# Performance work log

Measured on AMD Instinct MI355X. Metric: run time of the kernel, lower is better.

## Reference

```python
import jax, jax.numpy as jnp
import numpy as np

T = 131072          # signal length == RIR length
C = 4               # audio channels (torch code requires batch == 1)
SAMPLE_RATE = 16000
RT60 = 0.8          # 'large' room


def setup_inputs() -> dict:
    key = jax.random.key(0)
    k_audio, k_rir = jax.random.split(key)
    audio = jax.random.normal(k_audio, (1, C, T), dtype=jnp.float32)
    # synthetic RIR: exponentially decaying white noise, direct-path impulse at t=0
    t = jnp.arange(T, dtype=jnp.float32)
    decay = jnp.exp(-6.9 * t / (RT60 * SAMPLE_RATE))
    rir = jax.random.normal(k_rir, (T,), dtype=jnp.float32) * decay
    rir = rir.at[0].set(1.0)
    return {"audio": audio, "rir": rir}


def reference(audio, rir):
    # torch F.conv1d with padding = K-1 computes FULL cross-correlation:
    #   out[n] = sum_j audio[n-(K-1)+j] * rir[j],  n = 0..T+K-2
    # which equals full linear convolution of audio with flipped rir.
    # Implemented via zero-padded rFFT (mathematically identical, O(N log N)).
    L = audio.shape[-1] + rir.shape[-1] - 1          # 2T-1
    A = jnp.fft.rfft(audio, n=L, axis=-1)            # (1, C, Lf)
    K = jnp.fft.rfft(rir[::-1], n=L)                 # (Lf,)
    out = jnp.fft.irfft(A * K, n=L, axis=-1)         # (1, C, 2T-1)
    return out.astype(audio.dtype)
```

## Files before the change

kernel.cpp:

```cpp
#include <hip/hip_runtime.h>


#define NTOT 262144
#define TLEN 131072
#define PI2_N    2.3968449808418217e-5f
#define PI2_1024 6.1359231515425649e-3f
#define PI2_256  2.4543692606170260e-2f
#define LB(i) ((i) + ((i) >> 3))

__device__ __forceinline__ float2 cadd(float2 a, float2 b) { return make_float2(a.x + b.x, a.y + b.y); }
__device__ __forceinline__ float2 csub(float2 a, float2 b) { return make_float2(a.x - b.x, a.y - b.y); }
__device__ __forceinline__ float2 cmul(float2 a, float2 b) {
    return make_float2(a.x * b.x - a.y * b.y, a.x * b.y + a.y * b.x);
}
__device__ __forceinline__ float2 cmulc(float2 a, float2 b) {
    return make_float2(a.x * b.x + a.y * b.y, a.y * b.x - a.x * b.y);
}
__device__ __forceinline__ float2 cexp_(float ang) {
    float s, c;
    __sincosf(ang, &s, &c);
    return make_float2(c, s);
}

constexpr float CW16[16] = { 1.f, 0.92387953f, 0.70710678f, 0.38268343f, 0.f, -0.38268343f,
                             -0.70710678f, -0.92387953f, -1.f, -0.92387953f, -0.70710678f,
                             -0.38268343f, 0.f, 0.38268343f, 0.70710678f, 0.92387953f };
constexpr float SW16[16] = { 0.f, 0.38268343f, 0.70710678f, 0.92387953f, 1.f, 0.92387953f,
                             0.70710678f, 0.38268343f, 0.f, -0.38268343f, -0.70710678f,
                             -0.92387953f, -1.f, -0.92387953f, -0.70710678f, -0.38268343f };

template<int SIGN>
__device__ __forceinline__ void dft4(float2 x[4]) {
    float2 s0 = cadd(x[0], x[2]), d0 = csub(x[0], x[2]);
    float2 s1 = cadd(x[1], x[3]), d1 = csub(x[1], x[3]);
    float2 jd1 = (SIGN > 0) ? make_float2(-d1.y, d1.x) : make_float2(d1.y, -d1.x);
    x[0] = cadd(s0, s1);
    x[1] = cadd(d0, jd1);
    x[2] = csub(s0, s1);
    x[3] = csub(d0, jd1);
}

template<int SIGN, bool HZ>
__device__ __forceinline__ void dft16(float2 x[16]) {
    float2 A[4][4];
#pragma unroll
    for (int m0 = 0; m0 < 4; ++m0) {
        float2 g[4];
        if (HZ) {
            float2 a = x[m0], b = x[m0 + 4];
            float2 jb = (SIGN > 0) ? make_float2(-b.y, b.x) : make_float2(b.y, -b.x);
            g[0] = cadd(a, b);
            g[1] = cadd(a, jb);
            g[2] = csub(a, b);
            g[3] = csub(a, jb);
        } else {
            g[0] = x[m0]; g[1] = x[m0 + 4]; g[2] = x[m0 + 8]; g[3] = x[m0 + 12];
            dft4<SIGN>(g);
        }
#pragma unroll
        for (int j = 0; j < 4; ++j) {
            int k = (m0 * j) & 15;
            float2 w = make_float2(CW16[k], (SIGN < 0) ? -SW16[k] : SW16[k]);
            A[m0][j] = (m0 && j) ? cmul(g[j], w) : g[j];
        }
    }
#pragma unroll
    for (int j = 0; j < 4; ++j) {
        float2 g[4];
#pragma unroll
        for (int m0 = 0; m0 < 4; ++m0) g[m0] = A[m0][j];
        dft4<SIGN>(g);
#pragma unroll
        for (int l = 0; l < 4; ++l) x[j + 4 * l] = g[l];
    }
}

template<int SIGN>
__device__ __forceinline__ void twtab4(float2 x[4], int base, const float2* __restrict__ tab) {
#pragma unroll
    for (int i = 1; i < 4; ++i) {
        float2 w = tab[base * i];
        x[i] = (SIGN < 0) ? cmul(x[i], w) : cmulc(x[i], w);
    }
}

template<int SIGN>
__device__ void fft1024(float2 x[4], int t, float2* L0, float2* L1,
                        const float2* __restrict__ tab) {
    dft4<SIGN>(x);
    twtab4<SIGN>(x, t, tab);
#pragma unroll
    for (int i = 0; i < 4; ++i) L0[LB(4 * t + i)] = x[i];
    __syncthreads();
    {
        int q = t & 3, p = t >> 2;
#pragma unroll
        for (int i = 0; i < 4; ++i) x[i] = L0[LB(q + 4 * p + 256 * i)];
        dft4<SIGN>(x);
        twtab4<SIGN>(x, 4 * p, tab);
#pragma unroll
        for (int i = 0; i < 4; ++i) L1[LB(q + 16 * p + 4 * i)] = x[i];
    }
    __syncthreads();
    {
        int q = t & 15, p = t >> 4;
#pragma unroll
        for (int i = 0; i < 4; ++i) x[i] = L1[LB(q + 16 * p + 256 * i)];
        dft4<SIGN>(x);
        twtab4<SIGN>(x, 16 * p, tab);
#pragma unroll
        for (int i = 0; i < 4; ++i) L0[LB(q + 64 * p + 16 * i)] = x[i];
    }
    __syncthreads();
    {
        int q = t & 63, p = t >> 6;
#pragma unroll
        for (int i = 0; i < 4; ++i) x[i] = L0[LB(q + 64 * p + 256 * i)];
        dft4<SIGN>(x);
        twtab4<SIGN>(x, 64 * p, tab);
#pragma unroll
        for (int i = 0; i < 4; ++i) L1[LB(q + 256 * p + 64 * i)] = x[i];
    }
    __syncthreads();
#pragma unroll
    for (int i = 0; i < 4; ++i) x[i] = L1[LB(t + 256 * i)];
    dft4<SIGN>(x);
}

__global__ void __launch_bounds__(256) ka(const float* __restrict__ audio,
                                          const float* __restrict__ rir,
                                          float2* __restrict__ A1,
                                          float2* __restrict__ tab) {
    __shared__ float2 lds[256 * 17];
    const int bid = blockIdx.x;
    const int tid = threadIdx.x;
    const int c = tid & 15;
    const int t = tid >> 4;

    if (bid < 4)
        tab[bid * 256 + tid] = cexp_(-PI2_1024 * (float)(bid * 256 + tid));

    const int seq = bid >> 6;
    const int n2 = ((bid & 63) << 4) + c;

    float2 g[16];
    if (seq < 2) {
        const float* c0 = audio + (size_t)(2 * seq) * TLEN;
        const float* c1 = c0 + TLEN;
#pragma unroll
        for (int v = 0; v < 8; ++v) {
            int n = ((t + 16 * v) << 10) + n2;
            g[v] = make_float2(c0[n], c1[n]);
        }
    } else {
#pragma unroll
        for (int v = 0; v < 8; ++v) {
            int n = ((t + 16 * v) << 10) + n2;
            g[v] = make_float2(rir[TLEN - 1 - n], 0.f);
        }
    }

    dft16<-1, true>(g);
#pragma unroll
    for (int r = 1; r < 16; ++r)
        g[r] = cmul(g[r], cexp_(-PI2_256 * (float)(t * r)));
    if (t) g[0] = g[0];
#pragma unroll
    for (int r = 0; r < 16; ++r) lds[(r * 16 + t) * 17 + c] = g[r];
    __syncthreads();
#pragma unroll
    for (int u = 0; u < 16; ++u) g[u] = lds[(t * 16 + u) * 17 + c];

    dft16<-1, false>(g);

    float2* dst = A1 + ((size_t)seq << 18) + n2;
#pragma unroll
    for (int r = 0; r < 16; ++r) {
        int k1 = t + 16 * r;
        float2 v = cmul(g[r], cexp_(-PI2_N * (float)(n2 * k1)));
        dst[(size_t)k1 << 10] = v;
    }
}

__global__ void __launch_bounds__(256) kbf(const float2* __restrict__ A1,
                                           float2* __restrict__ Spec,
                                           const float2* __restrict__ tab) {
    __shared__ float2 L0[1152], L1[1152];
    const int t = threadIdx.x;
    const float2* src = A1 + ((size_t)blockIdx.x << 10);
    float2 x[4];
#pragma unroll
    for (int i = 0; i < 4; ++i) x[i] = src[t + 256 * i];
    fft1024<-1>(x, t, L0, L1, tab);
    float2* dst = Spec + ((size_t)blockIdx.x << 10) + t;
#pragma unroll
    for (int i = 0; i < 4; ++i) dst[256 * i] = x[i];
}

__global__ void __launch_bounds__(256) kbi(const float2* __restrict__ Spec,
                                           float2* __restrict__ D,
                                           const float2* __restrict__ tab) {
    __shared__ float2 L0[1152], L1[1152];
    const int t = threadIdx.x;
    const int k1 = blockIdx.x & 255;

    const float2* sz = Spec + ((size_t)blockIdx.x << 10);
    const float2* sr = Spec + ((size_t)(512 + k1) << 10);
    float2 x[4], r4[4];
#pragma unroll
    for (int i = 0; i < 4; ++i) x[i] = sz[t + 256 * i];
#pragma unroll
    for (int i = 0; i < 4; ++i) r4[i] = sr[t + 256 * i];

    const float invN = 3.814697265625e-6f;
#pragma unroll
    for (int i = 0; i < 4; ++i) {
        float2 y = cmul(x[i], r4[i]);
        x[i] = make_float2(y.x * invN, y.y * invN);
    }

    fft1024<1>(x, t, L0, L1, tab);

    float2 w  = cexp_(PI2_N * (float)(t * k1));
    float2 st = make_float2(tab[k1].x, -tab[k1].y);
    float2* d = D + ((size_t)blockIdx.x << 10) + t;
#pragma unroll
    for (int i = 0; i < 4; ++i) {
        d[256 * i] = cmul(x[i], w);
        w = cmul(w, st);
    }
}

__global__ void __launch_bounds__(256) kc(const float2* __restrict__ D,
                                          float* __restrict__ out, int Lout) {
    __shared__ float2 lds[256 * 17];
    const int bid = blockIdx.x;
    const int tid = threadIdx.x;
    const int c = tid & 15;
    const int t = tid >> 4;
    const int z = bid >> 6;
    const int n2 = ((bid & 63) << 4) + c;

    const float2* src = D + ((size_t)z << 18) + n2;
    float2 g[16];
#pragma unroll
    for (int v = 0; v < 16; ++v)
        g[v] = src[(size_t)(t + 16 * v) << 10];

    dft16<1, false>(g);
#pragma unroll
    for (int r = 1; r < 16; ++r)
        g[r] = cmul(g[r], cexp_(PI2_256 * (float)(t * r)));
#pragma unroll
    for (int r = 0; r < 16; ++r) lds[(r * 16 + t) * 17 + c] = g[r];
    __syncthreads();
#pragma unroll
    for (int u = 0; u < 16; ++u) g[u] = lds[(t * 16 + u) * 17 + c];

    dft16<1, false>(g);

    float* o0 = out + (size_t)(2 * z) * Lout;
    float* o1 = o0 + Lout;
#pragma unroll
    for (int r = 0; r < 16; ++r) {
        int n = ((t + 16 * r) << 10) + n2;
        if (n < Lout) { o0[n] = g[r].x; o1[n] = g[r].y; }
    }
}

extern "C" void kernel_launch(void* const* d_in, const int* in_sizes, int n_in,
                              void* d_out, int out_size, void* d_ws, size_t ws_size,
                              hipStream_t stream) {
    const float* audio = (const float*)d_in[0];
    const float* rir   = (const float*)d_in[1];
    float* out = (float*)d_out;
    int Lout = out_size / 4;

    float2* A1   = (float2*)d_ws;
    float2* Spec = A1 + 3 * NTOT;
    float2* D    = Spec + 3 * NTOT;
    float2* tab  = D + 2 * NTOT;

    ka <<<192, 256, 0, stream>>>(audio, rir, A1, tab);
    kbf<<<768, 256, 0, stream>>>(A1, Spec, tab);
    kbi<<<512, 256, 0, stream>>>(Spec, D, tab);
    kc <<<128, 256, 0, stream>>>(D, out, Lout);
}
```

Before: 24.83 us.

## Fuse forward column FFT into pointwise-multiply inverse FFT kernel

Merges the forward 1024-point FFT stage into the inverse-stage kernel. Each block now transforms its own audio row and the matching RIR row before multiplying, so the separate kernel launch and the Spec round trip through global memory go away. In exchange, the RIR row FFT is recomputed once per audio channel pair (twice per row instead of once), and each block does two more FFTs in sequence.

```diff
diff --git a/kernel.cpp b/kernel.cpp
--- a/kernel.cpp
+++ b/kernel.cpp
@@ -164,7 +164,6 @@
 #pragma unroll
     for (int r = 1; r < 16; ++r)
         g[r] = cmul(g[r], cexp_(-PI2_256 * (float)(t * r)));
-    if (t) g[0] = g[0];
 #pragma unroll
     for (int r = 0; r < 16; ++r) lds[(r * 16 + t) * 17 + c] = g[r];
     __syncthreads();
@@ -182,35 +181,23 @@
     }
 }
 
-__global__ void __launch_bounds__(256) kbf(const float2* __restrict__ A1,
-                                           float2* __restrict__ Spec,
-                                           const float2* __restrict__ tab) {
-    __shared__ float2 L0[1152], L1[1152];
-    const int t = threadIdx.x;
-    const float2* src = A1 + ((size_t)blockIdx.x << 10);
-    float2 x[4];
-#pragma unroll
-    for (int i = 0; i < 4; ++i) x[i] = src[t + 256 * i];
-    fft1024<-1>(x, t, L0, L1, tab);
-    float2* dst = Spec + ((size_t)blockIdx.x << 10) + t;
-#pragma unroll
-    for (int i = 0; i < 4; ++i) dst[256 * i] = x[i];
-}
-
-__global__ void __launch_bounds__(256) kbi(const float2* __restrict__ Spec,
-                                           float2* __restrict__ D,
-                                           const float2* __restrict__ tab) {
+__global__ void __launch_bounds__(256) kb(const float2* __restrict__ A1,
+                                          float2* __restrict__ D,
+                                          const float2* __restrict__ tab) {
     __shared__ float2 L0[1152], L1[1152];
     const int t = threadIdx.x;
     const int k1 = blockIdx.x & 255;
 
-    const float2* sz = Spec + ((size_t)blockIdx.x << 10);
-    const float2* sr = Spec + ((size_t)(512 + k1) << 10);
+    const float2* sz = A1 + ((size_t)blockIdx.x << 10);
+    const float2* sr = A1 + ((size_t)(512 + k1) << 10);
     float2 x[4], r4[4];
 #pragma unroll
     for (int i = 0; i < 4; ++i) x[i] = sz[t + 256 * i];
 #pragma unroll
     for (int i = 0; i < 4; ++i) r4[i] = sr[t + 256 * i];
+
+    fft1024<-1>(r4, t, L0, L1, tab);
+    fft1024<-1>(x, t, L0, L1, tab);
 
     const float invN = 3.814697265625e-6f;
 #pragma unroll
@@ -276,13 +263,11 @@
     float* out = (float*)d_out;
     int Lout = out_size / 4;
 
-    float2* A1   = (float2*)d_ws;
-    float2* Spec = A1 + 3 * NTOT;
-    float2* D    = Spec + 3 * NTOT;
-    float2* tab  = D + 2 * NTOT;
-
-    ka <<<192, 256, 0, stream>>>(audio, rir, A1, tab);
-    kbf<<<768, 256, 0, stream>>>(A1, Spec, tab);
-    kbi<<<512, 256, 0, stream>>>(Spec, D, tab);
-    kc <<<128, 256, 0, stream>>>(D, out, Lout);
-}
+    float2* A1  = (float2*)d_ws;
+    float2* D   = A1 + 3 * NTOT;
+    float2* tab = D + 2 * NTOT;
+
+    ka<<<192, 256, 0, stream>>>(audio, rir, A1, tab);
+    kb<<<512, 256, 0, stream>>>(A1, D, tab);
+    kc<<<128, 256, 0, stream>>>(D, out, Lout);
+}
```

Result: faster. 22.62 us (-8.9%).
